# Kernel tuning notes

Measured on AMD Instinct MI355X. Metric: run time of the kernel, lower is better.

## Reference

```python
import jax, jax.numpy as jnp
import numpy as np

B, S, H = 1, 2048, 4096
NH, NKV = 32, 8          # query heads, kv heads (GQA group = 4)
HD, VHD = 128, 128       # qk head_dim, v head_dim
ROPE = 64                # partial rotary dim (head_dim * 0.5)
NEG = -1e9


def setup_inputs() -> dict:
    key = jax.random.key(0)
    ks = jax.random.split(key, 6)
    hidden_states = jax.random.normal(ks[0], (B, S, H), dtype=jnp.float32)
    # real rotary embeddings, shape [1,1,S,ROPE] so they broadcast over heads
    inv_freq = 1.0 / (10000.0 ** (jnp.arange(0, ROPE, 2, dtype=jnp.float32) / ROPE))
    freqs = jnp.arange(S, dtype=jnp.float32)[:, None] * inv_freq[None, :]  # [S, ROPE/2]
    emb = jnp.concatenate([freqs, freqs], axis=-1)                          # [S, ROPE]
    cos = jnp.cos(emb)[None, None]  # [1,1,S,ROPE]
    sin = jnp.sin(emb)[None, None]
    # additive causal mask [1,1,S,S]
    causal = jnp.tril(jnp.ones((S, S), dtype=bool))
    attention_mask = jnp.where(causal, 0.0, NEG)[None, None].astype(jnp.float32)
    w_scale = 0.02
    Wq = jax.random.normal(ks[1], (H, NH * HD), dtype=jnp.float32) * w_scale
    Wk = jax.random.normal(ks[2], (H, NKV * HD), dtype=jnp.float32) * w_scale
    Wv = jax.random.normal(ks[3], (H, NKV * VHD), dtype=jnp.float32) * w_scale
    Wo = jax.random.normal(ks[4], (NH * VHD, H), dtype=jnp.float32) * w_scale
    sinks = jax.random.normal(ks[5], (NH,), dtype=jnp.float32)
    return {"hidden_states": hidden_states, "cos": cos, "sin": sin,
            "attention_mask": attention_mask, "Wq": Wq, "Wk": Wk, "Wv": Wv,
            "Wo": Wo, "sinks": sinks}


def _rotate_half(x):
    h = x.shape[-1] // 2
    return jnp.concatenate([-x[..., h:], x[..., :h]], axis=-1)


def reference(hidden_states, cos, sin, attention_mask, Wq, Wk, Wv, Wo, sinks):
    b, s, _ = hidden_states.shape
    scaling = HD ** -0.5
    # projections -> [b, heads, s, d]
    q = (hidden_states @ Wq).reshape(b, s, NH, HD).transpose(0, 2, 1, 3)
    k = (hidden_states @ Wk).reshape(b, s, NKV, HD).transpose(0, 2, 1, 3)
    v = (hidden_states @ Wv).reshape(b, s, NKV, VHD).transpose(0, 2, 1, 3)
    # partial RoPE on the first ROPE dims
    q_r, q_n = q[..., :ROPE], q[..., ROPE:]
    k_r, k_n = k[..., :ROPE], k[..., ROPE:]
    q_r = q_r * cos + _rotate_half(q_r) * sin
    k_r = k_r * cos + _rotate_half(k_r) * sin
    q = jnp.concatenate([q_r, q_n], axis=-1)
    k = jnp.concatenate([k_r, k_n], axis=-1)
    # GQA: repeat kv heads (repeat_interleave along head dim)
    n_rep = NH // NKV
    k = jnp.repeat(k, n_rep, axis=1)  # [b, NH, s, HD]
    v = jnp.repeat(v, n_rep, axis=1)  # [b, NH, s, VHD]
    scores = jnp.einsum('bhqd,bhkd->bhqk', q, k) * scaling + attention_mask
    # attention sinks: extra logit column per head, dropped after softmax
    sink_col = jnp.broadcast_to(sinks.reshape(1, NH, 1, 1), (b, NH, s, 1))
    logits = jnp.concatenate([scores, sink_col], axis=-1)
    w = jax.nn.softmax(logits.astype(jnp.float32), axis=-1).astype(q.dtype)[..., :-1]
    attn = jnp.einsum('bhqk,bhkd->bhqd', w, v)          # [b, NH, s, VHD]
    attn = attn.transpose(0, 2, 1, 3).reshape(b, s, NH * VHD)
    return attn @ Wo
```

## Files before the change

kernel.cpp:

```cpp
#include <hip/hip_runtime.h>
#include <hip/hip_bf16.h>
#include <cstdint>
#include <cstddef>

#define S_LEN 2048
#define NHEADS 32
#define NKVH   8
#define HDIM   128

using bf16x8 = __attribute__((ext_vector_type(8))) short;
using f32x4  = __attribute__((ext_vector_type(4))) float;
using f32x16 = __attribute__((ext_vector_type(16))) float;

__device__ __forceinline__ short f2bf(float f) {
  union { float f; unsigned u; } a; a.f = f;
  unsigned u = a.u;
  unsigned r = u + 0x7fffu + ((u >> 16) & 1u);
  return (short)(r >> 16);
}
__device__ __forceinline__ unsigned pack_bf2(float lo, float hi) {
  union { float f; unsigned u; } a, b; a.f = lo; b.f = hi;
  return __builtin_amdgcn_perm(b.u, a.u, 0x07060302);
}

__device__ __forceinline__ void gld16(const void* g, void* l) {
  __builtin_amdgcn_global_load_lds((__attribute__((address_space(1))) void*)(void*)g,
                                   (__attribute__((address_space(3))) void*)l, 16, 0, 0);
}

#define VMWAIT(N) asm volatile("s_waitcnt vmcnt(" #N ")" ::: "memory")
#define SCHEDB()  __builtin_amdgcn_sched_barrier(0)
#define MFMA16(a, b, c) __builtin_amdgcn_mfma_f32_16x16x32_bf16((a), (b), (c), 0, 0, 0)

__global__ void cvt_f32_bf16(const float* __restrict__ x, short* __restrict__ y, int n4) {
  int i = blockIdx.x * blockDim.x + threadIdx.x;
  if (i >= n4) return;
  float4 v = reinterpret_cast<const float4*>(x)[i];
  short4 o;
  o.x = f2bf(v.x); o.y = f2bf(v.y); o.z = f2bf(v.z); o.w = f2bf(v.w);
  reinterpret_cast<short4*>(y)[i] = o;
}

__global__ __launch_bounds__(256)
void transpose_to_bf16(const float* __restrict__ W, short* __restrict__ Wt,
                       int K, int N) {
  __shared__ float tile[32 * 33];
  const int bn = blockIdx.x * 32, bk = blockIdx.y * 32;
  const int t = threadIdx.x;
  const int c4 = t & 7, kr = t >> 3;
  float4 v = *(const float4*)&W[(size_t)(bk + kr) * N + bn + c4 * 4];
  tile[kr * 33 + c4 * 4 + 0] = v.x;
  tile[kr * 33 + c4 * 4 + 1] = v.y;
  tile[kr * 33 + c4 * 4 + 2] = v.z;
  tile[kr * 33 + c4 * 4 + 3] = v.w;
  __syncthreads();
  const int k4 = t & 7, nr = t >> 3;
  short4 o;
  o.x = f2bf(tile[(k4 * 4 + 0) * 33 + nr]);
  o.y = f2bf(tile[(k4 * 4 + 1) * 33 + nr]);
  o.z = f2bf(tile[(k4 * 4 + 2) * 33 + nr]);
  o.w = f2bf(tile[(k4 * 4 + 3) * 33 + nr]);
  *(short4*)&Wt[(size_t)(bn + nr) * K + bk + k4 * 4] = o;
}

#define QKV_TILE(TT, VM1, VM3, S12, S34) {                                         \
    const short* Ar = smem + ((TT) & 1) * 16384;                                   \
    const short* Br = smem + 32768 + ((TT) & 1) * 16384;                           \
    VMWAIT(VM1);                                                                   \
    __builtin_amdgcn_s_barrier();                                                  \
    SCHEDB();                                                                      \
    bf16x8 af[8], b0, b1;                                                          \
    _Pragma("unroll") for (int i = 0; i < 8; ++i)                                  \
      af[i] = *(const bf16x8*)&Ar[(wm + i * 16 + lr) * 32 + csw];                  \
    b0 = *(const bf16x8*)&Br[(wn +  0 + lr) * 32 + csw];                           \
    b1 = *(const bf16x8*)&Br[(wn + 16 + lr) * 32 + csw];                           \
    if (S12) stageA((TT) + 1, 1);                                                  \
    __builtin_amdgcn_s_setprio(1);                                                 \
    _Pragma("unroll") for (int i = 0; i < 8; ++i) {                                \
      acc[i][0] = MFMA16(af[i], b0, acc[i][0]);                                    \
      acc[i][1] = MFMA16(af[i], b1, acc[i][1]);                                    \
    }                                                                              \
    __builtin_amdgcn_s_setprio(0);                                                 \
    b0 = *(const bf16x8*)&Br[(wn + 32 + lr) * 32 + csw];                           \
    b1 = *(const bf16x8*)&Br[(wn + 48 + lr) * 32 + csw];                           \
    if (S12) stageB((TT) + 1, 1);                                                  \
    __builtin_amdgcn_s_setprio(1);                                                 \
    _Pragma("unroll") for (int i = 0; i < 8; ++i) {                                \
      acc[i][2] = MFMA16(af[i], b0, acc[i][2]);                                    \
      acc[i][3] = MFMA16(af[i], b1, acc[i][3]);                                    \
    }                                                                              \
    __builtin_amdgcn_s_setprio(0);                                                 \
    VMWAIT(VM3);                                                                   \
    __builtin_amdgcn_s_barrier();                                                  \
    SCHEDB();                                                                      \
    const short* Ar1 = Ar + 8192;                                                  \
    const short* Br1 = Br + 8192;                                                  \
    _Pragma("unroll") for (int i = 0; i < 8; ++i)                                  \
      af[i] = *(const bf16x8*)&Ar1[(wm + i * 16 + lr) * 32 + csw];                 \
    b0 = *(const bf16x8*)&Br1[(wn +  0 + lr) * 32 + csw];                          \
    b1 = *(const bf16x8*)&Br1[(wn + 16 + lr) * 32 + csw];                          \
    if (S34) stageA((TT) + 2, 0);                                                  \
    __builtin_amdgcn_s_setprio(1);                                                 \
    _Pragma("unroll") for (int i = 0; i < 8; ++i) {                                \
      acc[i][0] = MFMA16(af[i], b0, acc[i][0]);                                    \
      acc[i][1] = MFMA16(af[i], b1, acc[i][1]);                                    \
    }                                                                              \
    __builtin_amdgcn_s_setprio(0);                                                 \
    b0 = *(const bf16x8*)&Br1[(wn + 32 + lr) * 32 + csw];                          \
    b1 = *(const bf16x8*)&Br1[(wn + 48 + lr) * 32 + csw];                          \
    if (S34) stageB((TT) + 2, 0);                                                  \
    __builtin_amdgcn_s_setprio(1);                                                 \
    _Pragma("unroll") for (int i = 0; i < 8; ++i) {                                \
      acc[i][2] = MFMA16(af[i], b0, acc[i][2]);                                    \
      acc[i][3] = MFMA16(af[i], b1, acc[i][3]);                                    \
    }                                                                              \
    __builtin_amdgcn_s_setprio(0);                                                 \
  }

__global__ __launch_bounds__(512, 2)
void gemm_qkv(const short* __restrict__ A, const short* __restrict__ B,
              short* __restrict__ Qb, short* __restrict__ Kb, short* __restrict__ Vtb,
              const float* __restrict__ cosb, const float* __restrict__ sinb) {
  const int K = 4096;
  extern __shared__ __align__(16) short smem[];
  const int bn = blockIdx.x * 256;
  const int bm = blockIdx.y * 256;
  const int t = threadIdx.x;
  const int lane = t & 63;
  const int w = t >> 6;
  const int wm = (w >> 2) * 128;
  const int wn = (w & 3) * 64;
  const int lr = lane & 15;
  const int l4 = lane >> 4;
  const int csw = ((l4 ^ ((lr >> 1) & 3)) * 8);

  f32x4 acc[8][4] = {};

  const int srow0 = w * 16 + (lane >> 2);
  const int srow1 = (8 + w) * 16 + (lane >> 2);
  const int sch   = ((lane & 3) ^ ((lane >> 3) & 3)) * 8;
  const size_t ga0 = (size_t)(bm + srow0) * K + sch;
  const size_t ga1 = (size_t)(bm + srow1) * K + sch;
  const size_t gb0 = (size_t)(bn + srow0) * K + sch;
  const size_t gb1 = (size_t)(bn + srow1) * K + sch;
  const int ldl0 = w * 512 + lane * 8;
  const int ldl1 = (8 + w) * 512 + lane * 8;

  auto stageA = [&](int kt, int kh) {
    const int ko = kt * 64 + kh * 32;
    short* rb = smem + (kt & 1) * 16384 + kh * 8192;
    gld16(A + ga0 + ko, rb + ldl0);
    gld16(A + ga1 + ko, rb + ldl1);
  };
  auto stageB = [&](int kt, int kh) {
    const int ko = kt * 64 + kh * 32;
    short* rb = smem + 32768 + (kt & 1) * 16384 + kh * 8192;
    gld16(B + gb0 + ko, rb + ldl0);
    gld16(B + gb1 + ko, rb + ldl1);
  };

  stageA(0, 0); stageB(0, 0);
  stageA(0, 1); stageB(0, 1);
  stageA(1, 0); stageB(1, 0);

  for (int kt = 0; kt < 62; ++kt) QKV_TILE(kt, 8, 8, 1, 1);
  QKV_TILE(62, 8, 8, 1, 0);
  QKV_TILE(63, 4, 0, 0, 0);

  const int cr = (lane >> 4) << 2;
  const int cc = lane & 15;
  const int region = (bn >= 5120) ? 2 : (bn >= 4096 ? 1 : 0);

  if (region < 2) {
    if ((wn & 64) == 0) {
#pragma unroll
      for (int i = 0; i < 8; ++i) {
#pragma unroll
        for (int r = 0; r < 4; ++r) {
          int srow = bm + wm + i * 16 + cr + r;
#pragma unroll
          for (int j = 0; j < 2; ++j) {
            int c = j * 16 + cc;
            float cv = cosb[srow * 64 + c];
            float sv = sinb[srow * 64 + c];
            float x1 = acc[i][j][r], x2 = acc[i][j + 2][r];
            acc[i][j][r]     = x1 * cv - x2 * sv;
            acc[i][j + 2][r] = x2 * cv + x1 * sv;
          }
        }
      }
    }
#pragma unroll
    for (int i = 0; i < 8; ++i)
#pragma unroll
      for (int j = 0; j < 4; ++j) {
        int row = bm + wm + i * 16 + cr;
        int col = bn + wn + j * 16 + cc;
#pragma unroll
        for (int r = 0; r < 4; ++r) {
          short v = f2bf(acc[i][j][r]);
          if (region == 0) Qb[(size_t)(row + r) * 4096 + col] = v;
          else             Kb[(size_t)(row + r) * 1024 + (col - 4096)] = v;
        }
      }
  } else {
    __syncthreads();
#pragma unroll
    for (int h = 0; h < 2; ++h) {
      if ((wm >> 7) == h) {
#pragma unroll
        for (int i = 0; i < 8; ++i)
#pragma unroll
          for (int j = 0; j < 4; ++j) {
            int lc = wn + j * 16 + cc;
            int lrow = i * 16 + cr;
#pragma unroll
            for (int r = 0; r < 4; ++r)
              smem[lc * 132 + lrow + r] = f2bf(acc[i][j][r]);
          }
      }
      __syncthreads();
      int colx = t >> 1;
      int off = (t & 1) * 64;
      short* dst = Vtb + (size_t)(bn - 5120 + colx) * 2048 + bm + h * 128 + off;
#pragma unroll
      for (int c8 = 0; c8 < 8; ++c8)
        *(bf16x8*)(dst + c8 * 8) = *(const bf16x8*)&smem[colx * 132 + off + c8 * 8];
      if (h == 0) __syncthreads();
    }
  }
}

__global__ __launch_bounds__(256, 2)
void gemm_out(const short* __restrict__ A, const short* __restrict__ B,
              float* __restrict__ C) {
  const int K = 4096, N = 4096;
  __shared__ short smem[32768];
  const int bn = blockIdx.x * 128;
  const int bm = blockIdx.y * 128;
  const int t = threadIdx.x;
  const int lane = t & 63;
  const int wave = t >> 6;
  const int wm = (wave >> 1) * 64;
  const int wn = (wave & 1) * 64;
  const int lr = lane & 15;
  const int lk3 = lane >> 4;

  f32x4 acc[4][4] = {};

  const int srow = t >> 3;
  const int sch = (t & 7) ^ ((t >> 3) & 7);
  const size_t ab = (size_t)(bm + srow) * K + sch * 8;
  const size_t bb = (size_t)(bn + srow) * K + sch * 8;

  auto stage = [&](int k0, int b) {
    short* dst = smem + b * 16384 + t * 8;
#pragma unroll
    for (int p = 0; p < 4; ++p) {
      gld16(A + ab + k0 + (size_t)(p * 32) * K, dst + p * 2048);
      gld16(B + bb + k0 + (size_t)(p * 32) * K, dst + 8192 + p * 2048);
    }
  };

  stage(0, 0);
  for (int it = 0; it < 64; ++it) {
    __syncthreads();
    if (it + 1 < 64) stage((it + 1) * 64, (it + 1) & 1);
    const short* Asb = smem + (it & 1) * 16384;
    const short* Bsb = Asb + 8192;
#pragma unroll
    for (int h = 0; h < 2; ++h) {
      bf16x8 af[4], bfr[4];
#pragma unroll
      for (int i = 0; i < 4; ++i) {
        int row = wm + i * 16 + lr;
        af[i] = *(const bf16x8*)&Asb[row * 64 + (((h * 4 + lk3) ^ (lr & 7)) * 8)];
      }
#pragma unroll
      for (int j = 0; j < 4; ++j) {
        int row = wn + j * 16 + lr;
        bfr[j] = *(const bf16x8*)&Bsb[row * 64 + (((h * 4 + lk3) ^ (lr & 7)) * 8)];
      }
#pragma unroll
      for (int i = 0; i < 4; ++i)
#pragma unroll
        for (int j = 0; j < 4; ++j)
          acc[i][j] = __builtin_amdgcn_mfma_f32_16x16x32_bf16(af[i], bfr[j], acc[i][j], 0, 0, 0);
    }
  }

  const int cr = (lane >> 4) << 2;
  const int cc = lane & 15;
#pragma unroll
  for (int i = 0; i < 4; ++i)
#pragma unroll
    for (int j = 0; j < 4; ++j) {
      int row = bm + wm + i * 16 + cr;
      int col = bn + wn + j * 16 + cc;
#pragma unroll
      for (int r = 0; r < 4; ++r)
        C[(size_t)(row + r) * N + col] = acc[i][j][r];
    }
}

__global__ __launch_bounds__(256, 2)
void attn_kernel(const short* __restrict__ Q, const short* __restrict__ Kg,
                 const short* __restrict__ Vg, const float* __restrict__ sinks,
                 short* __restrict__ O) {
  __shared__ short lds[32768];
  const int h = blockIdx.x;
  const int qt = 15 - blockIdx.y;
  const int q0 = qt * 128;
  const int kvh = h >> 2;
  const int t = threadIdx.x;
  const int lane = t & 63;
  const int w = t >> 6;
  const int l31 = lane & 31;
  const int l7 = lane & 7;
  const bool qh = lane >= 32;
  const int q5 = qh ? 1 : 0;
  const int nkt = 2 * qt + 2;

  const int kch = (t & 15) ^ ((t >> 4) & 7);
  const short* kgb = Kg + (size_t)(t >> 4) * 1024 + kvh * 128 + kch * 8;
  const int vch = (t & 7) ^ ((t >> 3) & 7);
  const short* vgb = Vg + (size_t)(kvh * 128 + (t >> 3)) * 2048 + vch * 8;

  auto stage = [&](int kt, int b) {
    short* kl = lds + b * 16384 + t * 8;
    short* vl = lds + b * 16384 + 8192 + t * 8;
    const short* kg = kgb + (size_t)kt * 64 * 1024;
    const short* vg = vgb + kt * 64;
#pragma unroll
    for (int c = 0; c < 4; ++c) {
      gld16(kg + (size_t)c * 16 * 1024, kl + c * 2048);
      gld16(vg + (size_t)c * 32 * 2048, vl + c * 2048);
    }
  };

  const short* qp = Q + (size_t)(q0 + w * 32 + l31) * 4096 + h * 128 + q5 * 8;
  bf16x8 qf[8];
#pragma unroll
  for (int st = 0; st < 8; ++st) qf[st] = *(const bf16x8*)(qp + st * 16);

  union { short s[8]; bf16x8 v; } ones;
#pragma unroll
  for (int i = 0; i < 8; ++i) ones.s[i] = (short)0x3F80;

  f32x16 acc[4] = {};
  f32x16 lacc = {};

  stage(0, 0);
  const int qg = q0 + w * 32 + l31;
  const float ce = 0.12751743f;

  for (int kt = 0; kt < nkt; ++kt) {
    const int b = kt & 1;
    __syncthreads();
    if (kt + 1 < nkt) stage(kt + 1, b ^ 1);
    const short* Ks = lds + b * 16384;
    const short* Vs = Ks + 8192;

    f32x16 sa0 = {}, sa1 = {};
#pragma unroll
    for (int st = 0; st < 8; ++st) {
      const int cp = ((st * 2 + q5) ^ l7) * 8;
      bf16x8 k0 = *(const bf16x8*)(Ks + (l31) * 128 + cp);
      bf16x8 k1 = *(const bf16x8*)(Ks + (32 + l31) * 128 + cp);
      sa0 = __builtin_amdgcn_mfma_f32_32x32x16_bf16(k0, qf[st], sa0, 0, 0, 0);
      sa1 = __builtin_amdgcn_mfma_f32_32x32x16_bf16(k1, qf[st], sa1, 0, 0, 0);
    }

    if (kt >= 2 * qt) {
      const int kb0 = kt * 64 + q5 * 4;
#pragma unroll
      for (int r = 0; r < 16; ++r) {
        int kg0 = kb0 + ((r >> 2) << 3) + (r & 3);
        float s0 = (kg0 <= qg) ? sa0[r] * ce : -INFINITY;
        float s1 = (kg0 + 32 <= qg) ? sa1[r] * ce : -INFINITY;
        sa0[r] = __builtin_amdgcn_exp2f(s0);
        sa1[r] = __builtin_amdgcn_exp2f(s1);
      }
    } else {
#pragma unroll
      for (int r = 0; r < 16; ++r) {
        sa0[r] = __builtin_amdgcn_exp2f(sa0[r] * ce);
        sa1[r] = __builtin_amdgcn_exp2f(sa1[r] * ce);
      }
    }

#pragma unroll
    for (int s = 0; s < 4; ++s) {
      const f32x16& S = (s & 2) ? sa1 : sa0;
      float a0, a1, a2, a3, b0, b1, b2, b3;
      if (s & 1) {
        a0 = qh ? S[12] : S[8];  a1 = qh ? S[13] : S[9];
        a2 = qh ? S[14] : S[10]; a3 = qh ? S[15] : S[11];
        b0 = qh ? S[8]  : S[12]; b1 = qh ? S[9]  : S[13];
        b2 = qh ? S[10] : S[14]; b3 = qh ? S[11] : S[15];
      } else {
        a0 = qh ? S[4] : S[0]; a1 = qh ? S[5] : S[1];
        a2 = qh ? S[6] : S[2]; a3 = qh ? S[7] : S[3];
        b0 = qh ? S[0] : S[4]; b1 = qh ? S[1] : S[5];
        b2 = qh ? S[2] : S[6]; b3 = qh ? S[3] : S[7];
      }
      unsigned d0 = pack_bf2(a0, a1), d1 = pack_bf2(a2, a3);
      unsigned e0 = pack_bf2(b0, b1), e1 = pack_bf2(b2, b3);
      unsigned r0 = (unsigned)__shfl_xor((int)e0, 32, 64);
      unsigned r1 = (unsigned)__shfl_xor((int)e1, 32, 64);
      union { unsigned u[4]; bf16x8 v; } P;
      P.u[0] = qh ? r0 : d0;  P.u[1] = qh ? r1 : d1;
      P.u[2] = qh ? d0 : r0;  P.u[3] = qh ? d1 : r1;

      lacc = __builtin_amdgcn_mfma_f32_32x32x16_bf16(ones.v, P.v, lacc, 0, 0, 0);
#pragma unroll
      for (int m = 0; m < 4; ++m) {
        bf16x8 vf = *(const bf16x8*)(Vs + (m * 32 + l31) * 64 + (((s * 2 + q5) ^ l7) * 8));
        acc[m] = __builtin_amdgcn_mfma_f32_32x32x16_bf16(vf, P.v, acc[m], 0, 0, 0);
      }
    }
  }

  float denom = lacc[0] + __builtin_amdgcn_exp2f(sinks[h] * 1.4426950f);
  float rinv = 1.0f / denom;

  __syncthreads();
#pragma unroll
  for (int m = 0; m < 4; ++m) {
#pragma unroll
    for (int r = 0; r < 16; ++r) {
      int d = m * 32 + ((r >> 2) << 3) + q5 * 4 + (r & 3);
      int ql = w * 32 + l31;
      lds[ql * 128 + (((d >> 3) ^ l7) << 3) + (d & 7)] = f2bf(acc[m][r] * rinv);
    }
  }
  __syncthreads();
  const int qrow = t >> 1;
  const int half = (t & 1) * 8;
  short* ob = O + (size_t)(q0 + qrow) * 4096 + h * 128;
#pragma unroll
  for (int cc = 0; cc < 8; ++cc) {
    int chunk = half + cc;
    bf16x8 v = *(const bf16x8*)&lds[qrow * 128 + ((chunk ^ (qrow & 7)) << 3)];
    *(bf16x8*)(ob + chunk * 8) = v;
  }
}

extern "C" void kernel_launch(void* const* d_in, const int* in_sizes, int n_in,
                              void* d_out, int out_size, void* d_ws, size_t ws_size,
                              hipStream_t stream) {
  const float* hs    = (const float*)d_in[0];
  const float* cosb  = (const float*)d_in[1];
  const float* sinb  = (const float*)d_in[2];
  const float* Wq    = (const float*)d_in[4];
  const float* Wk    = (const float*)d_in[5];
  const float* Wv    = (const float*)d_in[6];
  const float* Wo    = (const float*)d_in[7];
  const float* sinks = (const float*)d_in[8];
  float* out = (float*)d_out;

  static bool attr_done = false;
  if (!attr_done) {
    hipFuncSetAttribute(reinterpret_cast<const void*>(&gemm_qkv),
                        hipFuncAttributeMaxDynamicSharedMemorySize, 131072);
    attr_done = true;
  }

  char* ws = (char*)d_ws;
  short* Xb    = (short*)ws;
  short* Wqkvt = (short*)(ws + 16777216);
  short* Qb    = (short*)(ws + 67108864);
  short* Kb    = (short*)(ws + 83886080);
  short* Vtb   = (short*)(ws + 88080384);
  short* Ab    = Xb;
  short* Wot   = Wqkvt;

  cvt_f32_bf16<<<8192, 256, 0, stream>>>(hs, Xb, 2097152);
  transpose_to_bf16<<<dim3(128, 128), 256, 0, stream>>>(Wq, Wqkvt, 4096, 4096);
  transpose_to_bf16<<<dim3(32, 128), 256, 0, stream>>>(Wk, Wqkvt + (size_t)4096 * 4096, 4096, 1024);
  transpose_to_bf16<<<dim3(32, 128), 256, 0, stream>>>(Wv, Wqkvt + (size_t)5120 * 4096, 4096, 1024);

  gemm_qkv<<<dim3(24, 8), 512, 131072, stream>>>(Xb, Wqkvt, Qb, Kb, Vtb, cosb, sinb);

  transpose_to_bf16<<<dim3(128, 128), 256, 0, stream>>>(Wo, Wot, 4096, 4096);

  attn_kernel<<<dim3(32, 16), 256, 0, stream>>>(Qb, Kb, Vtb, sinks, Ab);

  gemm_out<<<dim3(32, 16), 256, 0, stream>>>(Ab, Wot, out);
}
```

Measured before the change: 461.2 us.

## Fuse Wo transpose into QKV GEMM grid and restructure per-phase barriers

Adds 64 extra blocks to the QKV GEMM launch that transpose and convert Wo to bf16, so this work runs on CUs left idle by the 192-block GEMM grid instead of as a separate kernel launch. The fused path needs a separate workspace region and only runs when the workspace is large enough. The GEMM k-loop is also re-synchronised: barriers with lgkmcnt waits now surround each MFMA phase, and the vmcnt waits move to the end of each half-tile. The extra barriers add synchronisation overhead, and the transpose blocks compete with GEMM blocks for memory bandwidth.

```diff
diff --git a/kernel.cpp b/kernel.cpp
--- a/kernel.cpp
+++ b/kernel.cpp
@@ -29,6 +29,7 @@
 }
 
 #define VMWAIT(N) asm volatile("s_waitcnt vmcnt(" #N ")" ::: "memory")
+#define LGKM0()   asm volatile("s_waitcnt lgkmcnt(0)" ::: "memory")
 #define SCHEDB()  __builtin_amdgcn_sched_barrier(0)
 #define MFMA16(a, b, c) __builtin_amdgcn_mfma_f32_16x16x32_bf16((a), (b), (c), 0, 0, 0)
 
@@ -63,36 +64,36 @@
   *(short4*)&Wt[(size_t)(bn + nr) * K + bk + k4 * 4] = o;
 }
 
-#define QKV_TILE(TT, VM1, VM3, S12, S34) {                                         \
+#define QKV_PH_MFMA(J0, J1, B0, B1)                                                \
+    __builtin_amdgcn_s_setprio(1);                                                 \
+    _Pragma("unroll") for (int i = 0; i < 8; ++i) {                                \
+      acc[i][J0] = MFMA16(af[i], B0, acc[i][J0]);                                  \
+      acc[i][J1] = MFMA16(af[i], B1, acc[i][J1]);                                  \
+    }                                                                              \
+    __builtin_amdgcn_s_setprio(0);
+
+#define QKV_TILE(TT, S12, S34, VMA, VMB) {                                         \
     const short* Ar = smem + ((TT) & 1) * 16384;                                   \
     const short* Br = smem + 32768 + ((TT) & 1) * 16384;                           \
-    VMWAIT(VM1);                                                                   \
-    __builtin_amdgcn_s_barrier();                                                  \
-    SCHEDB();                                                                      \
     bf16x8 af[8], b0, b1;                                                          \
+                                                 \
     _Pragma("unroll") for (int i = 0; i < 8; ++i)                                  \
       af[i] = *(const bf16x8*)&Ar[(wm + i * 16 + lr) * 32 + csw];                  \
     b0 = *(const bf16x8*)&Br[(wn +  0 + lr) * 32 + csw];                           \
     b1 = *(const bf16x8*)&Br[(wn + 16 + lr) * 32 + csw];                           \
     if (S12) stageA((TT) + 1, 1);                                                  \
-    __builtin_amdgcn_s_setprio(1);                                                 \
-    _Pragma("unroll") for (int i = 0; i < 8; ++i) {                                \
-      acc[i][0] = MFMA16(af[i], b0, acc[i][0]);                                    \
-      acc[i][1] = MFMA16(af[i], b1, acc[i][1]);                                    \
-    }                                                                              \
-    __builtin_amdgcn_s_setprio(0);                                                 \
+    __builtin_amdgcn_s_barrier(); LGKM0(); SCHEDB();                               \
+    QKV_PH_MFMA(0, 1, b0, b1)                                                      \
+    __builtin_amdgcn_s_barrier(); SCHEDB();                                        \
+                                                         \
     b0 = *(const bf16x8*)&Br[(wn + 32 + lr) * 32 + csw];                           \
     b1 = *(const bf16x8*)&Br[(wn + 48 + lr) * 32 + csw];                           \
     if (S12) stageB((TT) + 1, 1);                                                  \
-    __builtin_amdgcn_s_setprio(1);                                                 \
-    _Pragma("unroll") for (int i = 0; i < 8; ++i) {                                \
-      acc[i][2] = MFMA16(af[i], b0, acc[i][2]);                                    \
-      acc[i][3] = MFMA16(af[i], b1, acc[i][3]);                                    \
-    }                                                                              \
-    __builtin_amdgcn_s_setprio(0);                                                 \
-    VMWAIT(VM3);                                                                   \
-    __builtin_amdgcn_s_barrier();                                                  \
-    SCHEDB();                                                                      \
+    __builtin_amdgcn_s_barrier(); LGKM0(); SCHEDB();                               \
+    QKV_PH_MFMA(2, 3, b0, b1)                                                      \
+    VMWAIT(VMA);                                                                   \
+    __builtin_amdgcn_s_barrier(); SCHEDB();                                        \
+                                                 \
     const short* Ar1 = Ar + 8192;                                                  \
     const short* Br1 = Br + 8192;                                                  \
     _Pragma("unroll") for (int i = 0; i < 8; ++i)                                  \
@@ -100,31 +101,58 @@
     b0 = *(const bf16x8*)&Br1[(wn +  0 + lr) * 32 + csw];                          \
     b1 = *(const bf16x8*)&Br1[(wn + 16 + lr) * 32 + csw];                          \
     if (S34) stageA((TT) + 2, 0);                                                  \
-    __builtin_amdgcn_s_setprio(1);                                                 \
-    _Pragma("unroll") for (int i = 0; i < 8; ++i) {                                \
-      acc[i][0] = MFMA16(af[i], b0, acc[i][0]);                                    \
-      acc[i][1] = MFMA16(af[i], b1, acc[i][1]);                                    \
-    }                                                                              \
-    __builtin_amdgcn_s_setprio(0);                                                 \
+    __builtin_amdgcn_s_barrier(); LGKM0(); SCHEDB();                               \
+    QKV_PH_MFMA(0, 1, b0, b1)                                                      \
+    __builtin_amdgcn_s_barrier(); SCHEDB();                                        \
+                                                         \
     b0 = *(const bf16x8*)&Br1[(wn + 32 + lr) * 32 + csw];                          \
     b1 = *(const bf16x8*)&Br1[(wn + 48 + lr) * 32 + csw];                          \
     if (S34) stageB((TT) + 2, 0);                                                  \
-    __builtin_amdgcn_s_setprio(1);                                                 \
-    _Pragma("unroll") for (int i = 0; i < 8; ++i) {                                \
-      acc[i][2] = MFMA16(af[i], b0, acc[i][2]);                                    \
-      acc[i][3] = MFMA16(af[i], b1, acc[i][3]);                                    \
-    }                                                                              \
-    __builtin_amdgcn_s_setprio(0);                                                 \
+    __builtin_amdgcn_s_barrier(); LGKM0(); SCHEDB();                               \
+    QKV_PH_MFMA(2, 3, b0, b1)                                                      \
+    VMWAIT(VMB);                                                                   \
+    __builtin_amdgcn_s_barrier(); SCHEDB();                                        \
   }
 
 __global__ __launch_bounds__(512, 2)
 void gemm_qkv(const short* __restrict__ A, const short* __restrict__ B,
               short* __restrict__ Qb, short* __restrict__ Kb, short* __restrict__ Vtb,
-              const float* __restrict__ cosb, const float* __restrict__ sinb) {
+              const float* __restrict__ cosb, const float* __restrict__ sinb,
+              const float* __restrict__ Wo, short* __restrict__ Wot) {
   const int K = 4096;
   extern __shared__ __align__(16) short smem[];
-  const int bn = blockIdx.x * 256;
-  const int bm = blockIdx.y * 256;
+  const int bid = blockIdx.x;
+
+  if (bid >= 192) {
+    const int bidt = bid - 192;
+    float* tl = (float*)smem;
+    const int t = threadIdx.x;
+    const int hb = t >> 8;
+    const int tt = t & 255;
+    float* tile = tl + hb * (32 * 33);
+    const int c4 = tt & 7, kr = tt >> 3;
+    for (int it = 0; it < 128; ++it) {
+      const int tau = it * 128 + bidt * 2 + hb;
+      const int bn = (tau & 127) * 32, bk = (tau >> 7) * 32;
+      float4 v = *(const float4*)&Wo[(size_t)(bk + kr) * 4096 + bn + c4 * 4];
+      tile[kr * 33 + c4 * 4 + 0] = v.x;
+      tile[kr * 33 + c4 * 4 + 1] = v.y;
+      tile[kr * 33 + c4 * 4 + 2] = v.z;
+      tile[kr * 33 + c4 * 4 + 3] = v.w;
+      __syncthreads();
+      short4 o;
+      o.x = f2bf(tile[(c4 * 4 + 0) * 33 + kr]);
+      o.y = f2bf(tile[(c4 * 4 + 1) * 33 + kr]);
+      o.z = f2bf(tile[(c4 * 4 + 2) * 33 + kr]);
+      o.w = f2bf(tile[(c4 * 4 + 3) * 33 + kr]);
+      *(short4*)&Wot[(size_t)(bn + kr) * 4096 + bk + c4 * 4] = o;
+      __syncthreads();
+    }
+    return;
+  }
+
+  const int bn = (bid % 24) * 256;
+  const int bm = (bid / 24) * 256;
   const int t = threadIdx.x;
   const int lane = t & 63;
   const int w = t >> 6;
@@ -162,10 +190,12 @@
   stageA(0, 0); stageB(0, 0);
   stageA(0, 1); stageB(0, 1);
   stageA(1, 0); stageB(1, 0);
-
-  for (int kt = 0; kt < 62; ++kt) QKV_TILE(kt, 8, 8, 1, 1);
-  QKV_TILE(62, 8, 8, 1, 0);
-  QKV_TILE(63, 4, 0, 0, 0);
+  VMWAIT(8);
+  __builtin_amdgcn_s_barrier(); SCHEDB();
+
+  for (int kt = 0; kt < 62; ++kt) QKV_TILE(kt, 1, 1, 8, 8);
+  QKV_TILE(62, 1, 0, 8, 4);
+  QKV_TILE(63, 0, 0, 0, 0);
 
   const int cr = (lane >> 4) << 2;
   const int cc = lane & 15;
@@ -473,16 +503,20 @@
   short* Kb    = (short*)(ws + 83886080);
   short* Vtb   = (short*)(ws + 88080384);
   short* Ab    = Xb;
-  short* Wot   = Wqkvt;
+
+  const bool fuse_wo = ws_size >= (size_t)92274688 + 33554432;
+  short* Wot = fuse_wo ? (short*)(ws + 92274688) : Wqkvt;
 
   cvt_f32_bf16<<<8192, 256, 0, stream>>>(hs, Xb, 2097152);
   transpose_to_bf16<<<dim3(128, 128), 256, 0, stream>>>(Wq, Wqkvt, 4096, 4096);
   transpose_to_bf16<<<dim3(32, 128), 256, 0, stream>>>(Wk, Wqkvt + (size_t)4096 * 4096, 4096, 1024);
   transpose_to_bf16<<<dim3(32, 128), 256, 0, stream>>>(Wv, Wqkvt + (size_t)5120 * 4096, 4096, 1024);
 
-  gemm_qkv<<<dim3(24, 8), 512, 131072, stream>>>(Xb, Wqkvt, Qb, Kb, Vtb, cosb, sinb);
-
-  transpose_to_bf16<<<dim3(128, 128), 256, 0, stream>>>(Wo, Wot, 4096, 4096);
+  gemm_qkv<<<dim3(fuse_wo ? 256 : 192), 512, 131072, stream>>>(
+      Xb, Wqkvt, Qb, Kb, Vtb, cosb, sinb, Wo, Wot);
+
+  if (!fuse_wo)
+    transpose_to_bf16<<<dim3(128, 128), 256, 0, stream>>>(Wo, Wot, 4096, 4096);
 
   attn_kernel<<<dim3(32, 16), 256, 0, stream>>>(Qb, Kb, Vtb, sinks, Ab);
 
```

After: 468.8 us. No clear change (+1.7%).

## Merge preprocessing launches and overlap Wo transpose with QKV GEMM blocks

Applied to the files above, without the earlier changes.

Folds the hidden-state bf16 conversion and the Wq/Wk/Wv transposes into one preprocess kernel, removing three launches. It also appends 64 extra blocks to the QKV GEMM grid that transpose Wo into a separate workspace region, so this work runs concurrently with the GEMM instead of as its own launch. The fused path only runs when the workspace is large enough. The extra blocks compete with GEMM blocks for CUs and bandwidth and may lengthen the GEMM tail.

```diff
diff --git a/kernel.cpp b/kernel.cpp
--- a/kernel.cpp
+++ b/kernel.cpp
@@ -32,13 +32,49 @@
 #define SCHEDB()  __builtin_amdgcn_sched_barrier(0)
 #define MFMA16(a, b, c) __builtin_amdgcn_mfma_f32_16x16x32_bf16((a), (b), (c), 0, 0, 0)
 
-__global__ void cvt_f32_bf16(const float* __restrict__ x, short* __restrict__ y, int n4) {
-  int i = blockIdx.x * blockDim.x + threadIdx.x;
-  if (i >= n4) return;
-  float4 v = reinterpret_cast<const float4*>(x)[i];
+__global__ __launch_bounds__(256)
+void preprocess(const float* __restrict__ hs, short* __restrict__ Xb,
+                const float* __restrict__ Wq, const float* __restrict__ Wk,
+                const float* __restrict__ Wv, short* __restrict__ Wqkvt) {
+  __shared__ float tile[32 * 33];
+  int bid = blockIdx.x;
+  const int t = threadIdx.x;
+
+  if (bid < 8192) {
+    int i = bid * 256 + t;
+    float4 v = reinterpret_cast<const float4*>(hs)[i];
+    short4 o;
+    o.x = f2bf(v.x); o.y = f2bf(v.y); o.z = f2bf(v.z); o.w = f2bf(v.w);
+    reinterpret_cast<short4*>(Xb)[i] = o;
+    return;
+  }
+  bid -= 8192;
+  const float* W; short* Wt; int N, bn, bk;
+  if (bid < 16384) {
+    W = Wq; Wt = Wqkvt; N = 4096;
+    bn = (bid & 127) * 32; bk = (bid >> 7) * 32;
+  } else if (bid < 20480) {
+    bid -= 16384;
+    W = Wk; Wt = Wqkvt + (size_t)4096 * 4096; N = 1024;
+    bn = (bid & 31) * 32; bk = (bid >> 5) * 32;
+  } else {
+    bid -= 20480;
+    W = Wv; Wt = Wqkvt + (size_t)5120 * 4096; N = 1024;
+    bn = (bid & 31) * 32; bk = (bid >> 5) * 32;
+  }
+  const int c4 = t & 7, kr = t >> 3;
+  float4 v = *(const float4*)&W[(size_t)(bk + kr) * N + bn + c4 * 4];
+  tile[kr * 33 + c4 * 4 + 0] = v.x;
+  tile[kr * 33 + c4 * 4 + 1] = v.y;
+  tile[kr * 33 + c4 * 4 + 2] = v.z;
+  tile[kr * 33 + c4 * 4 + 3] = v.w;
+  __syncthreads();
   short4 o;
-  o.x = f2bf(v.x); o.y = f2bf(v.y); o.z = f2bf(v.z); o.w = f2bf(v.w);
-  reinterpret_cast<short4*>(y)[i] = o;
+  o.x = f2bf(tile[(c4 * 4 + 0) * 33 + kr]);
+  o.y = f2bf(tile[(c4 * 4 + 1) * 33 + kr]);
+  o.z = f2bf(tile[(c4 * 4 + 2) * 33 + kr]);
+  o.w = f2bf(tile[(c4 * 4 + 3) * 33 + kr]);
+  *(short4*)&Wt[(size_t)(bn + kr) * 4096 + bk + c4 * 4] = o;
 }
 
 __global__ __launch_bounds__(256)
@@ -120,11 +156,42 @@
 __global__ __launch_bounds__(512, 2)
 void gemm_qkv(const short* __restrict__ A, const short* __restrict__ B,
               short* __restrict__ Qb, short* __restrict__ Kb, short* __restrict__ Vtb,
-              const float* __restrict__ cosb, const float* __restrict__ sinb) {
+              const float* __restrict__ cosb, const float* __restrict__ sinb,
+              const float* __restrict__ Wo, short* __restrict__ Wot) {
   const int K = 4096;
   extern __shared__ __align__(16) short smem[];
-  const int bn = blockIdx.x * 256;
-  const int bm = blockIdx.y * 256;
+  const int bid = blockIdx.x;
+
+  if (bid >= 192) {
+    const int bidt = bid - 192;
+    float* tl = (float*)smem;
+    const int t = threadIdx.x;
+    const int hb = t >> 8;
+    const int tt = t & 255;
+    float* tile = tl + hb * (32 * 33);
+    const int c4 = tt & 7, kr = tt >> 3;
+    for (int it = 0; it < 128; ++it) {
+      const int tau = it * 128 + bidt * 2 + hb;
+      const int bn = (tau & 127) * 32, bk = (tau >> 7) * 32;
+      float4 v = *(const float4*)&Wo[(size_t)(bk + kr) * 4096 + bn + c4 * 4];
+      tile[kr * 33 + c4 * 4 + 0] = v.x;
+      tile[kr * 33 + c4 * 4 + 1] = v.y;
+      tile[kr * 33 + c4 * 4 + 2] = v.z;
+      tile[kr * 33 + c4 * 4 + 3] = v.w;
+      __syncthreads();
+      short4 o;
+      o.x = f2bf(tile[(c4 * 4 + 0) * 33 + kr]);
+      o.y = f2bf(tile[(c4 * 4 + 1) * 33 + kr]);
+      o.z = f2bf(tile[(c4 * 4 + 2) * 33 + kr]);
+      o.w = f2bf(tile[(c4 * 4 + 3) * 33 + kr]);
+      *(short4*)&Wot[(size_t)(bn + kr) * 4096 + bk + c4 * 4] = o;
+      __syncthreads();
+    }
+    return;
+  }
+
+  const int bn = (bid % 24) * 256;
+  const int bm = (bid / 24) * 256;
   const int t = threadIdx.x;
   const int lane = t & 63;
   const int w = t >> 6;
@@ -473,16 +540,17 @@
   short* Kb    = (short*)(ws + 83886080);
   short* Vtb   = (short*)(ws + 88080384);
   short* Ab    = Xb;
-  short* Wot   = Wqkvt;
-
-  cvt_f32_bf16<<<8192, 256, 0, stream>>>(hs, Xb, 2097152);
-  transpose_to_bf16<<<dim3(128, 128), 256, 0, stream>>>(Wq, Wqkvt, 4096, 4096);
-  transpose_to_bf16<<<dim3(32, 128), 256, 0, stream>>>(Wk, Wqkvt + (size_t)4096 * 4096, 4096, 1024);
-  transpose_to_bf16<<<dim3(32, 128), 256, 0, stream>>>(Wv, Wqkvt + (size_t)5120 * 4096, 4096, 1024);
-
-  gemm_qkv<<<dim3(24, 8), 512, 131072, stream>>>(Xb, Wqkvt, Qb, Kb, Vtb, cosb, sinb);
-
-  transpose_to_bf16<<<dim3(128, 128), 256, 0, stream>>>(Wo, Wot, 4096, 4096);
+
+  const bool fuse_wo = ws_size >= (size_t)92274688 + 33554432;
+  short* Wot = fuse_wo ? (short*)(ws + 92274688) : Wqkvt;
+
+  preprocess<<<32768, 256, 0, stream>>>(hs, Xb, Wq, Wk, Wv, Wqkvt);
+
+  gemm_qkv<<<dim3(fuse_wo ? 256 : 192), 512, 131072, stream>>>(
+      Xb, Wqkvt, Qb, Kb, Vtb, cosb, sinb, Wo, Wot);
+
+  if (!fuse_wo)
+    transpose_to_bf16<<<dim3(128, 128), 256, 0, stream>>>(Wo, Wot, 4096, 4096);
 
   attn_kernel<<<dim3(32, 16), 256, 0, stream>>>(Qb, Kb, Vtb, sinks, Ab);
 
```

Result: slower. 471.3 us (+2.2%).
